# Optimization experiments

Measured on AMD Instinct MI355X. Metric: run time of the kernel, lower is better.

## Reference

```python
import jax, jax.numpy as jnp
import numpy as np

N = 50000        # nodes
E = 1600000      # edges
NFEAT = 128      # node feature dim
NEDGE = 16       # raw edge feature dim
NHID = 128
NLAYER = 4
NGRAPH = 512
NOUT = 128
BN_EPS = 1e-5


def _bn(h, g, b):
    # eval-mode BatchNorm1d with running_mean=0, running_var=1
    return h * (g / jnp.sqrt(1.0 + BN_EPS)) + b


def setup_inputs() -> dict:
    key = jax.random.key(0)
    ks = jax.random.split(key, 24)
    s = 0.05
    inp = {
        "x": jax.random.normal(ks[0], (N, NFEAT), jnp.float32),
        "edge_index": jax.random.randint(ks[1], (2, E), 0, N, jnp.int64),
        "edge_attr": jax.random.normal(ks[2], (E, NEDGE), jnp.float32),
        "batch": jnp.sort(jax.random.randint(ks[3], (N,), 0, NGRAPH, jnp.int64)),
        # input encoder MLP (Linear + BN + ReLU)
        "in_W": jax.random.normal(ks[4], (NFEAT, NHID), jnp.float32) * s,
        "in_b": jnp.zeros((NHID,), jnp.float32),
        "in_g": jnp.ones((NHID,), jnp.float32),
        "in_beta": jnp.zeros((NHID,), jnp.float32),
        # per-layer edge encoder MLPs
        "edge_W": jax.random.normal(ks[5], (NLAYER, NEDGE, NHID), jnp.float32) * s,
        "edge_b": jnp.zeros((NLAYER, NHID), jnp.float32),
        "edge_g": jnp.ones((NLAYER, NHID), jnp.float32),
        "edge_beta": jnp.zeros((NLAYER, NHID), jnp.float32),
        # per-layer GINEConv linear (bias=False since bn=True) and eps
        "conv_W": jax.random.normal(ks[6], (NLAYER, NHID, NHID), jnp.float32) * s,
        "eps": jnp.zeros((NLAYER,), jnp.float32),
        # per-layer BatchNorm after conv
        "bn_g": jnp.ones((NLAYER, NHID), jnp.float32),
        "bn_b": jnp.zeros((NLAYER, NHID), jnp.float32),
        # output encoder: 2-layer MLP, norm after layer 1, no final activation
        "out_W1": jax.random.normal(ks[7], (NHID, NHID), jnp.float32) * s,
        "out_b1": jnp.zeros((NHID,), jnp.float32),
        "out_g1": jnp.ones((NHID,), jnp.float32),
        "out_beta1": jnp.zeros((NHID,), jnp.float32),
        "out_W2": jax.random.normal(ks[8], (NHID, NOUT), jnp.float32) * s,
        "out_b2": jnp.zeros((NOUT,), jnp.float32),
    }
    return inp


def reference(x, edge_index, edge_attr, batch,
              in_W, in_b, in_g, in_beta,
              edge_W, edge_b, edge_g, edge_beta,
              conv_W, eps, bn_g, bn_b,
              out_W1, out_b1, out_g1, out_beta1,
              out_W2, out_b2):
    # input encoder (MLP, 1 layer: Linear + BN + ReLU)
    h = jax.nn.relu(_bn(x @ in_W + in_b, in_g, in_beta))
    prev = h
    src, dst = edge_index[0], edge_index[1]
    for l in range(NLAYER):
        # edge encoder
        ea = jax.nn.relu(_bn(edge_attr @ edge_W[l] + edge_b[l], edge_g[l], edge_beta[l]))
        # GINEConv: messages relu(x_src + e), sum-aggregate to dst
        m = jax.nn.relu(h[src] + ea)                         # [E, NHID]
        agg = jax.ops.segment_sum(m, dst, num_segments=N)    # [N, NHID]
        h = ((1.0 + eps[l]) * h + agg) @ conv_W[l]
        h = jax.nn.relu(_bn(h, bn_g[l], bn_b[l]))            # dropout=0
        h = h + prev                                         # residual
        prev = h
    # add pooling over graphs
    pooled = jax.ops.segment_sum(h, batch, num_segments=NGRAPH)  # [NGRAPH, NHID]
    # output encoder: Linear+BN+ReLU, then Linear
    o = jax.nn.relu(_bn(pooled @ out_W1 + out_b1, out_g1, out_beta1))
    return o @ out_W2 + out_b2
```

## Files before the change

kernel.cpp:

```cpp
#include <hip/hip_runtime.h>
#include <stdint.h>

typedef uint32_t u32;
typedef _Float16 h2v __attribute__((ext_vector_type(2)));
typedef __attribute__((ext_vector_type(8))) short bf16x8;
typedef __attribute__((ext_vector_type(8))) _Float16 f16x8_t;
typedef __attribute__((ext_vector_type(4))) float f32x4;

#define NGRAPH 512

__device__ __forceinline__ float uif(u32 u) { return __builtin_bit_cast(float, u); }
__device__ __forceinline__ u32 fiu(float f) { return __builtin_bit_cast(u32, f); }
__device__ __forceinline__ unsigned short bf16r(float f) {
    return (unsigned short)((fiu(f) + 0x8000u) >> 16);
}
__device__ __forceinline__ u32 pack_bf16(float lo, float hi) {
    return ((fiu(lo) + 0x8000u) >> 16) | ((fiu(hi) + 0x8000u) & 0xFFFF0000u);
}
__device__ __forceinline__ u32 pkh(float a, float b) {
    unsigned short la = __builtin_bit_cast(unsigned short, (_Float16)a);
    unsigned short hb = __builtin_bit_cast(unsigned short, (_Float16)b);
    return (u32)la | ((u32)hb << 16);
}

__global__ __launch_bounds__(256) void prep_kernel(
    const float* __restrict__ in_b, const float* __restrict__ in_g, const float* __restrict__ in_beta,
    const float* __restrict__ edge_b, const float* __restrict__ edge_g, const float* __restrict__ edge_beta,
    const float* __restrict__ bn_g, const float* __restrict__ bn_b,
    const float* __restrict__ out_b1, const float* __restrict__ out_g1, const float* __restrict__ out_beta1,
    float* __restrict__ consts)
{
    int c = threadIdx.x;
    if (c >= 128) return;
    const float rs = rsqrtf(1.0f + 1e-5f);
    float es = in_g[c] * rs;
    consts[c]       = es;
    consts[128 + c] = in_b[c] * es + in_beta[c];
    for (int l = 0; l < 4; ++l) {
        float s = edge_g[l*128 + c] * rs;
        consts[256  + l*128 + c] = s;
        consts[768  + l*128 + c] = edge_b[l*128 + c] * s + edge_beta[l*128 + c];
        float bs = bn_g[l*128 + c] * rs;
        consts[1280 + l*128 + c] = bs;
        consts[1792 + l*128 + c] = bn_b[l*128 + c];
    }
    float s1 = out_g1[c] * rs;
    consts[2304 + c] = s1;
    consts[2432 + c] = out_b1[c] * s1 + out_beta1[c];
}

__global__ __launch_bounds__(256) void wfrag_kernel(
    const float* __restrict__ edge_W, _Float16* __restrict__ wfrag)
{
    int idx = blockIdx.x*blockDim.x + threadIdx.x;
    if (idx >= 4*8*64*8) return;
    int j = idx & 7, lane = (idx >> 3) & 63, t = (idx >> 9) & 7, l = idx >> 12;
    int k = (lane >> 4)*8 + j;
    int n = t*16 + (lane & 15);
    wfrag[idx] = (k < 16) ? (_Float16)edge_W[(l*16 + k)*128 + n] : (_Float16)0.f;
}

__global__ __launch_bounds__(256) void prepw_kernel(
    const float* __restrict__ in_W, const float* __restrict__ conv_W,
    unsigned short* __restrict__ WtAll)
{
    for (int idx = blockIdx.x*blockDim.x + threadIdx.x; idx < 5*128*128;
         idx += gridDim.x*blockDim.x) {
        int w = idx >> 14, rem = idx & 16383;
        int nn = rem >> 7, kk = rem & 127;
        const float* S = (w == 0) ? in_W : conv_W + (size_t)(w-1)*16384;
        WtAll[idx] = bf16r(S[kk*128 + nn]);
    }
}

__global__ __launch_bounds__(256) void xconv_kernel(
    const float* __restrict__ x, u32* __restrict__ x16, int n4)
{
    for (int i = blockIdx.x*blockDim.x + threadIdx.x; i < n4;
         i += gridDim.x*blockDim.x) {
        float4 v = *(const float4*)(x + (size_t)i*4);
        uint2 o; o.x = pack_bf16(v.x, v.y); o.y = pack_bf16(v.z, v.w);
        *(uint2*)(x16 + (size_t)i*2) = o;
    }
}

__global__ __launch_bounds__(256) void count_kernel(
    const int* __restrict__ dst, int E, int* __restrict__ cnt)
{
    for (int e = blockIdx.x*blockDim.x + threadIdx.x; e < E; e += gridDim.x*blockDim.x)
        atomicAdd(&cnt[dst[e]], 1);
}

__global__ __launch_bounds__(1024) void scan_kernel(
    const int* __restrict__ cnt, int n, int E,
    int* __restrict__ offs, int* __restrict__ cursor)
{
    __shared__ int sh[1024];
    const int t = threadIdx.x;
    const int chunk = (n + 1023) >> 10;
    const int lo = t * chunk;
    const int hi = min(n, lo + chunk);
    int s = 0;
    for (int i = lo; i < hi; ++i) s += cnt[i];
    sh[t] = s;
    __syncthreads();
    for (int d = 1; d < 1024; d <<= 1) {
        int v = (t >= d) ? sh[t - d] : 0;
        __syncthreads();
        sh[t] += v;
        __syncthreads();
    }
    int base = sh[t] - s;
    for (int i = lo; i < hi; ++i) { int c = cnt[i]; offs[i] = base; cursor[i] = base; base += c; }
    if (t == 1023) offs[n] = E;
}

__global__ __launch_bounds__(256) void scatter_kernel(
    const int* __restrict__ src, const int* __restrict__ dst,
    const float* __restrict__ attr, int E,
    int* __restrict__ cursor, int* __restrict__ srcoff, uint4* __restrict__ attrp)
{
    const int T = gridDim.x * blockDim.x;
    const int tid = blockIdx.x*blockDim.x + threadIdx.x;
    int e[4]; int p[4];
    #pragma unroll
    for (int k = 0; k < 4; ++k) e[k] = tid + k*T;
    #pragma unroll
    for (int k = 0; k < 4; ++k)
        if (e[k] < E) p[k] = atomicAdd(&cursor[dst[e[k]]], 1);
    #pragma unroll
    for (int k = 0; k < 4; ++k) {
        if (e[k] >= E) continue;
        const int ee = e[k], pp = p[k];
        srcoff[pp] = src[ee] * 256;
        const float4* ar = (const float4*)(attr + (size_t)ee*16);
        float4 v0 = ar[0], v1 = ar[1], v2 = ar[2], v3 = ar[3];
        uint4 o0, o1;
        o0.x = pkh(v0.x, v0.y); o0.y = pkh(v0.z, v0.w);
        o0.z = pkh(v1.x, v1.y); o0.w = pkh(v1.z, v1.w);
        o1.x = pkh(v2.x, v2.y); o1.y = pkh(v2.z, v2.w);
        o1.z = pkh(v3.x, v3.y); o1.w = pkh(v3.z, v3.w);
        attrp[2*(size_t)pp] = o0; attrp[2*(size_t)pp + 1] = o1;
    }
}

__global__ __launch_bounds__(256) void goff_kernel(
    const int* __restrict__ batch, int n, int* __restrict__ goff)
{
    int g = blockIdx.x*blockDim.x + threadIdx.x;
    if (g > NGRAPH) return;
    if (g == NGRAPH) { goff[NGRAPH] = n; return; }
    int lo = 0, hi = n;
    while (lo < hi) { int m = (lo + hi) >> 1; if (batch[m] < g) lo = m + 1; else hi = m; }
    goff[g] = lo;
}

__global__ __launch_bounds__(256) void agg_kernel(
    const char* __restrict__ hb,
    const uint4* __restrict__ attrp,
    const int* __restrict__ srcoff,
    const int* __restrict__ offs,
    const _Float16* __restrict__ wfrag,
    const float* __restrict__ escale, const float* __restrict__ eoff,
    const float* __restrict__ epsp, int layer,
    u32* __restrict__ C16, int n)
{
    __shared__ float eabuf[4][128];
    const int wave = threadIdx.x >> 6, lane = threadIdx.x & 63;
    const int lane4 = lane * 4;
    const int c0 = lane * 2;
    const int l15 = lane & 15, l4 = lane >> 4;

    f16x8_t bw[8];
    #pragma unroll
    for (int t = 0; t < 8; ++t)
        bw[t] = *(const f16x8_t*)(wfrag + ((size_t)(layer*8 + t)*64 + lane)*8);
    float sc[8], of[8];
    #pragma unroll
    for (int t = 0; t < 8; ++t) {
        sc[t] = escale[l15 + 16*t];
        of[t] = eoff[l15 + 16*t];
    }
    const float epsv = 1.0f + epsp[layer];
    const f16x8_t az = (f16x8_t)(_Float16)0.f;

    for (int node = blockIdx.x*4 + wave; node < n; node += gridDim.x*4) {
        const int beg = offs[node], end = offs[node+1];

        float easum[8];
        #pragma unroll
        for (int t = 0; t < 8; ++t) easum[t] = 0.f;
        for (int g = beg; g < end; g += 16) {
            const int rem = end - g;
            f16x8_t a = az;
            if (l4 < 2) {
                int e = g + l15; if (e > end - 1) e = end - 1;
                a = *(const f16x8_t*)((const char*)attrp + (size_t)e*32 + l4*16);
            }
            if (rem >= 16) {
                #pragma unroll
                for (int t = 0; t < 8; ++t) {
                    f32x4 d = __builtin_amdgcn_mfma_f32_16x16x32_f16(
                        a, bw[t], f32x4{0.f,0.f,0.f,0.f}, 0, 0, 0);
                    #pragma unroll
                    for (int r = 0; r < 4; ++r)
                        easum[t] += fmaxf(fmaf(d[r], sc[t], of[t]), 0.f);
                }
            } else {
                #pragma unroll
                for (int t = 0; t < 8; ++t) {
                    f32x4 d = __builtin_amdgcn_mfma_f32_16x16x32_f16(
                        a, bw[t], f32x4{0.f,0.f,0.f,0.f}, 0, 0, 0);
                    #pragma unroll
                    for (int r = 0; r < 4; ++r) {
                        float y = fmaxf(fmaf(d[r], sc[t], of[t]), 0.f);
                        easum[t] += ((l4*4 + r) < rem) ? y : 0.f;
                    }
                }
            }
        }
        #pragma unroll
        for (int t = 0; t < 8; ++t) {
            float v = easum[t];
            v += __shfl_xor(v, 16);
            v += __shfl_xor(v, 32);
            easum[t] = v;
        }
        if (l4 == 0) {
            #pragma unroll
            for (int t = 0; t < 8; ++t)
                eabuf[wave][t*16 + l15] = easum[t];
        }
        float2 ea2 = *(float2*)&eabuf[wave][c0];

        float acc0 = ea2.x, acc1 = ea2.y;
        auto hedge = [&](int idx) {
            const int iu = __builtin_amdgcn_readfirstlane(idx);
            const u32 hv = *(const u32*)(hb + srcoff[iu] + lane4);
            acc0 += uif(hv << 16);
            acc1 += uif(hv & 0xFFFF0000u);
        };
        int i = beg;
        for (; i + 1 < end; i += 2) { hedge(i); hedge(i + 1); }
        if (i < end) hedge(i);

        const u32 hn = *(const u32*)(hb + (size_t)node*256 + lane4);
        float t0 = fmaf(epsv, uif(hn << 16), acc0);
        float t1 = fmaf(epsv, uif(hn & 0xFFFF0000u), acc1);
        C16[(size_t)node*64 + lane] = pack_bf16(t0, t1);
    }
}

__global__ __launch_bounds__(256) void conv_mfma_kernel(
    const unsigned short* X16, int M,
    const unsigned short* __restrict__ Wt,
    const float* __restrict__ scale, const float* __restrict__ off,
    const unsigned short* __restrict__ resid16,
    unsigned short* out16, int do_relu)
{
    __shared__ unsigned short Ws[128*128];
    for (int i = threadIdx.x*8; i < 128*128; i += 256*8) {
        int row = i >> 7;
        int bo = (i & 127) * 2;
        int4 v = *(const int4*)(Wt + i);
        *(int4*)((char*)Ws + row*256 + (bo ^ ((row & 7) << 4))) = v;
    }
    __syncthreads();
    const int wave = threadIdx.x >> 6, lane = threadIdx.x & 63;
    const int row0 = blockIdx.x*64 + wave*16;
    const int l15 = lane & 15, l4 = lane >> 4;
    int arow = row0 + l15; if (arow > M-1) arow = M-1;
    const unsigned short* ap = X16 + (size_t)arow*128 + l4*8;
    f32x4 acc[8];
    #pragma unroll
    for (int t = 0; t < 8; ++t) acc[t] = f32x4{0.f, 0.f, 0.f, 0.f};
    #pragma unroll
    for (int ks = 0; ks < 4; ++ks) {
        bf16x8 a = *(const bf16x8*)(ap + ks*32);
        #pragma unroll
        for (int t = 0; t < 8; ++t) {
            int brow = t*16 + l15;
            int bo = ks*64 + l4*16;
            bf16x8 b = *(const bf16x8*)((const char*)Ws + brow*256 + (bo ^ ((brow & 7) << 4)));
            acc[t] = __builtin_amdgcn_mfma_f32_16x16x32_bf16(a, b, acc[t], 0, 0, 0);
        }
    }
    #pragma unroll
    for (int t = 0; t < 8; ++t) {
        int col = t*16 + l15;
        float sc = scale[col], of = off[col];
        #pragma unroll
        for (int r = 0; r < 4; ++r) {
            int row = row0 + l4*4 + r;
            if (row < M) {
                float y = fmaf(acc[t][r], sc, of);
                if (do_relu) y = fmaxf(y, 0.f);
                if (resid16) y += uif((u32)resid16[(size_t)row*128 + col] << 16);
                out16[(size_t)row*128 + col] = bf16r(y);
            }
        }
    }
}

__global__ __launch_bounds__(256) void pool_kernel(
    const u32* __restrict__ h16, const int* __restrict__ goff,
    float* __restrict__ pooled)
{
    const int wave = threadIdx.x >> 6, lane = threadIdx.x & 63;
    const int g = blockIdx.x*4 + wave;
    if (g >= NGRAPH) return;
    float ax = 0.f, ay = 0.f;
    const int beg = goff[g], end = goff[g+1];
    for (int node = beg; node < end; ++node) {
        u32 v = h16[(size_t)node*64 + lane];
        ax += uif(v << 16); ay += uif(v & 0xFFFF0000u);
    }
    *(float2*)&pooled[g*128 + lane*2] = make_float2(ax, ay);
}

__global__ __launch_bounds__(256) void gemm128_kernel(
    const float* __restrict__ in, int rows,
    const float* __restrict__ W,
    const float* __restrict__ scale, const float* __restrict__ off,
    float* out, int do_relu)
{
    __shared__ float Wsh[128*128];
    for (int i = threadIdx.x*4; i < 128*128; i += 256*4)
        *(float4*)&Wsh[i] = *(const float4*)&W[i];
    __syncthreads();
    const int wave = threadIdx.x >> 6, lane = threadIdx.x & 63;
    const int c0 = lane * 2;
    const float sc0 = scale ? scale[c0]   : 1.0f;
    const float sc1 = scale ? scale[c0+1] : 1.0f;
    const float of0 = off ? off[c0]   : 0.0f;
    const float of1 = off ? off[c0+1] : 0.0f;
    for (int rp = blockIdx.x*4 + wave; rp*2 < rows; rp += gridDim.x*4) {
        const int row0 = __builtin_amdgcn_readfirstlane(rp * 2);
        const float* xr = in + (size_t)row0 * 128;
        float a00 = 0.f, a01 = 0.f, a10 = 0.f, a11 = 0.f;
        #pragma unroll 8
        for (int k = 0; k < 128; ++k) {
            float x0 = xr[k];
            float x1 = xr[128 + k];
            float2 w = *(const float2*)&Wsh[k*128 + c0];
            a00 = fmaf(x0, w.x, a00); a01 = fmaf(x0, w.y, a01);
            a10 = fmaf(x1, w.x, a10); a11 = fmaf(x1, w.y, a11);
        }
        float y00 = fmaf(a00, sc0, of0), y01 = fmaf(a01, sc1, of1);
        float y10 = fmaf(a10, sc0, of0), y11 = fmaf(a11, sc1, of1);
        if (do_relu) {
            y00 = fmaxf(y00, 0.f); y01 = fmaxf(y01, 0.f);
            y10 = fmaxf(y10, 0.f); y11 = fmaxf(y11, 0.f);
        }
        *(float2*)&out[(size_t)row0*128 + c0]     = make_float2(y00, y01);
        *(float2*)&out[(size_t)(row0+1)*128 + c0] = make_float2(y10, y11);
    }
}

extern "C" void kernel_launch(void* const* d_in, const int* in_sizes, int n_in,
                              void* d_out, int out_size, void* d_ws, size_t ws_size,
                              hipStream_t stream)
{
    const float* x         = (const float*)d_in[0];
    const int*   eidx      = (const int*)d_in[1];
    const float* eattr     = (const float*)d_in[2];
    const int*   batch     = (const int*)d_in[3];
    const float* in_W      = (const float*)d_in[4];
    const float* in_b      = (const float*)d_in[5];
    const float* in_g      = (const float*)d_in[6];
    const float* in_beta   = (const float*)d_in[7];
    const float* edge_W    = (const float*)d_in[8];
    const float* edge_b    = (const float*)d_in[9];
    const float* edge_g    = (const float*)d_in[10];
    const float* edge_beta = (const float*)d_in[11];
    const float* conv_W    = (const float*)d_in[12];
    const float* epsp      = (const float*)d_in[13];
    const float* bn_g      = (const float*)d_in[14];
    const float* bn_b      = (const float*)d_in[15];
    const float* out_W1    = (const float*)d_in[16];
    const float* out_b1    = (const float*)d_in[17];
    const float* out_g1    = (const float*)d_in[18];
    const float* out_beta1 = (const float*)d_in[19];
    const float* out_W2    = (const float*)d_in[20];
    const float* out_b2    = (const float*)d_in[21];

    const int N = in_sizes[0] / 128;
    const int E = in_sizes[1] / 2;
    const int* src = eidx;
    const int* dst = eidx + E;

    char* ws = (char*)d_ws;
    size_t o = 0;
    auto alloc = [&](size_t bytes) { void* p = ws + o; o = (o + bytes + 255) & ~(size_t)255; return p; };
    unsigned short* P    = (unsigned short*)alloc((size_t)N * 128 * 2);
    unsigned short* Q    = (unsigned short*)alloc((size_t)N * 128 * 2);
    uint4* attrp         = (uint4*)alloc((size_t)E * 32);
    int*   srcoff        = (int*)alloc((size_t)E * 4);
    int*   offs          = (int*)alloc((size_t)(N + 1) * 4);
    int*   cursor        = (int*)alloc((size_t)N * 4);
    int*   cnt           = (int*)alloc((size_t)N * 4);
    int*   goff          = (int*)alloc((NGRAPH + 1) * 4);
    float* pooled        = (float*)alloc(NGRAPH * 128 * 4);
    float* o1            = (float*)alloc(NGRAPH * 128 * 4);
    float* consts        = (float*)alloc(2560 * 4);
    _Float16* wfrag      = (_Float16*)alloc(4 * 8 * 64 * 8 * 2);
    unsigned short* WtAll = (unsigned short*)alloc(5 * 128 * 128 * 2);

    prep_kernel<<<1, 256, 0, stream>>>(in_b, in_g, in_beta,
                                       edge_b, edge_g, edge_beta,
                                       bn_g, bn_b, out_b1, out_g1, out_beta1,
                                       consts);
    wfrag_kernel<<<64, 256, 0, stream>>>(edge_W, wfrag);
    prepw_kernel<<<80, 256, 0, stream>>>(in_W, conv_W, WtAll);
    xconv_kernel<<<2048, 256, 0, stream>>>(x, (u32*)Q, N * 32);

    (void)hipMemsetAsync(cnt, 0, (size_t)N * 4, stream);
    count_kernel<<<2048, 256, 0, stream>>>(dst, E, cnt);
    scan_kernel<<<1, 1024, 0, stream>>>(cnt, N, E, offs, cursor);
    scatter_kernel<<<2048, 256, 0, stream>>>(src, dst, eattr, E, cursor, srcoff, attrp);
    goff_kernel<<<3, 256, 0, stream>>>(batch, N, goff);

    const int gblocks = (N + 63) / 64;
    conv_mfma_kernel<<<gblocks, 256, 0, stream>>>(Q, N, WtAll,
                                                  consts, consts + 128,
                                                  nullptr, Q, 1);

    unsigned short* cur = Q;
    unsigned short* oth = P;
    for (int l = 0; l < 4; ++l) {
        agg_kernel<<<2048, 256, 0, stream>>>((const char*)cur, attrp, srcoff, offs,
                                             wfrag,
                                             consts + 256 + l*128,
                                             consts + 768 + l*128,
                                             epsp, l, (u32*)oth, N);
        conv_mfma_kernel<<<gblocks, 256, 0, stream>>>(oth, N,
                                                      WtAll + (size_t)(1 + l)*16384,
                                                      consts + 1280 + l*128,
                                                      consts + 1792 + l*128,
                                                      cur, oth, 1);
        unsigned short* t = cur; cur = oth; oth = t;
    }

    pool_kernel<<<128, 256, 0, stream>>>((const u32*)cur, goff, pooled);

    gemm128_kernel<<<64, 256, 0, stream>>>(pooled, NGRAPH, out_W1,
                                           consts + 2304, consts + 2432, o1, 1);
    gemm128_kernel<<<64, 256, 0, stream>>>(o1, NGRAPH, out_W2,
                                           nullptr, out_b2, (float*)d_out, 0);
}
```

Baseline: 970.7 us.

## Precompute all four layers' edge-encoder aggregates once, then gather-only per layer

```diff
diff --git a/kernel.cpp b/kernel.cpp
--- a/kernel.cpp
+++ b/kernel.cpp
@@ -50,14 +50,18 @@
 }
 
 __global__ __launch_bounds__(256) void wfrag_kernel(
-    const float* __restrict__ edge_W, _Float16* __restrict__ wfrag)
+    const float* __restrict__ edge_W, const float* __restrict__ edge_g,
+    _Float16* __restrict__ wfrag)
 {
     int idx = blockIdx.x*blockDim.x + threadIdx.x;
     if (idx >= 4*8*64*8) return;
     int j = idx & 7, lane = (idx >> 3) & 63, t = (idx >> 9) & 7, l = idx >> 12;
     int k = (lane >> 4)*8 + j;
     int n = t*16 + (lane & 15);
-    wfrag[idx] = (k < 16) ? (_Float16)edge_W[(l*16 + k)*128 + n] : (_Float16)0.f;
+    const float rs = rsqrtf(1.0f + 1e-5f);
+    wfrag[idx] = (k < 16)
+        ? (_Float16)(edge_W[(l*16 + k)*128 + n] * (edge_g[l*128 + n] * rs))
+        : (_Float16)0.f;
 }
 
 __global__ __launch_bounds__(256) void prepw_kernel(
@@ -155,41 +159,34 @@
     goff[g] = lo;
 }
 
-__global__ __launch_bounds__(256) void agg_kernel(
-    const char* __restrict__ hb,
-    const uint4* __restrict__ attrp,
-    const int* __restrict__ srcoff,
-    const int* __restrict__ offs,
-    const _Float16* __restrict__ wfrag,
-    const float* __restrict__ escale, const float* __restrict__ eoff,
-    const float* __restrict__ epsp, int layer,
-    u32* __restrict__ C16, int n)
+__global__ __launch_bounds__(256) void eagg4_kernel(
+    const uint4* __restrict__ attrp, const int* __restrict__ offs,
+    const _Float16* __restrict__ wfrag, const float* __restrict__ consts,
+    u32* __restrict__ eagg, int n)
 {
     __shared__ float eabuf[4][128];
     const int wave = threadIdx.x >> 6, lane = threadIdx.x & 63;
-    const int lane4 = lane * 4;
     const int c0 = lane * 2;
     const int l15 = lane & 15, l4 = lane >> 4;
 
-    f16x8_t bw[8];
-    #pragma unroll
-    for (int t = 0; t < 8; ++t)
-        bw[t] = *(const f16x8_t*)(wfrag + ((size_t)(layer*8 + t)*64 + lane)*8);
-    float sc[8], of[8];
-    #pragma unroll
-    for (int t = 0; t < 8; ++t) {
-        sc[t] = escale[l15 + 16*t];
-        of[t] = eoff[l15 + 16*t];
-    }
-    const float epsv = 1.0f + epsp[layer];
+    f16x8_t bw[32];
+    #pragma unroll
+    for (int lt = 0; lt < 32; ++lt)
+        bw[lt] = *(const f16x8_t*)(wfrag + ((size_t)lt*64 + lane)*8);
+    float of[32];
+    #pragma unroll
+    for (int l = 0; l < 4; ++l)
+        #pragma unroll
+        for (int t = 0; t < 8; ++t)
+            of[l*8 + t] = consts[768 + l*128 + t*16 + l15];
     const f16x8_t az = (f16x8_t)(_Float16)0.f;
 
     for (int node = blockIdx.x*4 + wave; node < n; node += gridDim.x*4) {
         const int beg = offs[node], end = offs[node+1];
-
-        float easum[8];
+        float easum[32];
         #pragma unroll
-        for (int t = 0; t < 8; ++t) easum[t] = 0.f;
+        for (int lt = 0; lt < 32; ++lt) easum[lt] = 0.f;
+
         for (int g = beg; g < end; g += 16) {
             const int rem = end - g;
             f16x8_t a = az;
@@ -199,54 +196,96 @@
             }
             if (rem >= 16) {
                 #pragma unroll
-                for (int t = 0; t < 8; ++t) {
+                for (int lt = 0; lt < 32; ++lt) {
                     f32x4 d = __builtin_amdgcn_mfma_f32_16x16x32_f16(
-                        a, bw[t], f32x4{0.f,0.f,0.f,0.f}, 0, 0, 0);
+                        a, bw[lt], f32x4{0.f,0.f,0.f,0.f}, 0, 0, 0);
                     #pragma unroll
                     for (int r = 0; r < 4; ++r)
-                        easum[t] += fmaxf(fmaf(d[r], sc[t], of[t]), 0.f);
+                        easum[lt] += fmaxf(d[r] + of[lt], 0.f);
                 }
             } else {
                 #pragma unroll
-                for (int t = 0; t < 8; ++t) {
+                for (int lt = 0; lt < 32; ++lt) {
                     f32x4 d = __builtin_amdgcn_mfma_f32_16x16x32_f16(
-                        a, bw[t], f32x4{0.f,0.f,0.f,0.f}, 0, 0, 0);
+                        a, bw[lt], f32x4{0.f,0.f,0.f,0.f}, 0, 0, 0);
                     #pragma unroll
                     for (int r = 0; r < 4; ++r) {
-                        float y = fmaxf(fmaf(d[r], sc[t], of[t]), 0.f);
-                        easum[t] += ((l4*4 + r) < rem) ? y : 0.f;
+                        float y = fmaxf(d[r] + of[lt], 0.f);
+                        easum[lt] += ((l4*4 + r) < rem) ? y : 0.f;
                     }
                 }
             }
         }
         #pragma unroll
-        for (int t = 0; t < 8; ++t) {
-            float v = easum[t];
-            v += __shfl_xor(v, 16);
-            v += __shfl_xor(v, 32);
-            easum[t] = v;
-        }
-        if (l4 == 0) {
+        for (int l = 0; l < 4; ++l) {
             #pragma unroll
-            for (int t = 0; t < 8; ++t)
-                eabuf[wave][t*16 + l15] = easum[t];
-        }
-        float2 ea2 = *(float2*)&eabuf[wave][c0];
-
-        float acc0 = ea2.x, acc1 = ea2.y;
-        auto hedge = [&](int idx) {
-            const int iu = __builtin_amdgcn_readfirstlane(idx);
-            const u32 hv = *(const u32*)(hb + srcoff[iu] + lane4);
-            acc0 += uif(hv << 16);
-            acc1 += uif(hv & 0xFFFF0000u);
-        };
+            for (int t = 0; t < 8; ++t) {
+                float v = easum[l*8 + t];
+                v += __shfl_xor(v, 16);
+                v += __shfl_xor(v, 32);
+                if (l4 == 0) eabuf[wave][t*16 + l15] = v;
+            }
+            float2 ea2 = *(float2*)&eabuf[wave][c0];
+            eagg[(size_t)l*n*64 + (size_t)node*64 + lane] = pack_bf16(ea2.x, ea2.y);
+        }
+    }
+}
+
+__global__ __launch_bounds__(256) void hagg_kernel(
+    const char* __restrict__ hb, const int* __restrict__ srcoff,
+    const int* __restrict__ offs, const u32* __restrict__ eagg_l,
+    const float* __restrict__ epsp, int layer,
+    u32* __restrict__ C16, int n)
+{
+    const int wave = threadIdx.x >> 6, lane = threadIdx.x & 63;
+    const int lane4 = lane * 4;
+    const float epsv = 1.0f + epsp[layer];
+    for (int node = blockIdx.x*4 + wave; node < n; node += gridDim.x*4) {
+        const int beg = offs[node], end = offs[node+1];
+        float acc0 = 0.f, acc1 = 0.f;
         int i = beg;
-        for (; i + 1 < end; i += 2) { hedge(i); hedge(i + 1); }
-        if (i < end) hedge(i);
-
+        for (; i + 7 < end; i += 8) {
+            const int iu = __builtin_amdgcn_readfirstlane(i);
+            const int4 sa = *(const int4*)(srcoff + iu);
+            const int4 sb = *(const int4*)(srcoff + iu + 4);
+            const u32 h0 = *(const u32*)(hb + sa.x + lane4);
+            const u32 h1 = *(const u32*)(hb + sa.y + lane4);
+            const u32 h2 = *(const u32*)(hb + sa.z + lane4);
+            const u32 h3 = *(const u32*)(hb + sa.w + lane4);
+            const u32 h4 = *(const u32*)(hb + sb.x + lane4);
+            const u32 h5 = *(const u32*)(hb + sb.y + lane4);
+            const u32 h6 = *(const u32*)(hb + sb.z + lane4);
+            const u32 h7 = *(const u32*)(hb + sb.w + lane4);
+            acc0 += uif(h0 << 16); acc1 += uif(h0 & 0xFFFF0000u);
+            acc0 += uif(h1 << 16); acc1 += uif(h1 & 0xFFFF0000u);
+            acc0 += uif(h2 << 16); acc1 += uif(h2 & 0xFFFF0000u);
+            acc0 += uif(h3 << 16); acc1 += uif(h3 & 0xFFFF0000u);
+            acc0 += uif(h4 << 16); acc1 += uif(h4 & 0xFFFF0000u);
+            acc0 += uif(h5 << 16); acc1 += uif(h5 & 0xFFFF0000u);
+            acc0 += uif(h6 << 16); acc1 += uif(h6 & 0xFFFF0000u);
+            acc0 += uif(h7 << 16); acc1 += uif(h7 & 0xFFFF0000u);
+        }
+        for (; i + 3 < end; i += 4) {
+            const int iu = __builtin_amdgcn_readfirstlane(i);
+            const int4 sa = *(const int4*)(srcoff + iu);
+            const u32 h0 = *(const u32*)(hb + sa.x + lane4);
+            const u32 h1 = *(const u32*)(hb + sa.y + lane4);
+            const u32 h2 = *(const u32*)(hb + sa.z + lane4);
+            const u32 h3 = *(const u32*)(hb + sa.w + lane4);
+            acc0 += uif(h0 << 16); acc1 += uif(h0 & 0xFFFF0000u);
+            acc0 += uif(h1 << 16); acc1 += uif(h1 & 0xFFFF0000u);
+            acc0 += uif(h2 << 16); acc1 += uif(h2 & 0xFFFF0000u);
+            acc0 += uif(h3 << 16); acc1 += uif(h3 & 0xFFFF0000u);
+        }
+        for (; i < end; ++i) {
+            const int iu = __builtin_amdgcn_readfirstlane(i);
+            const u32 h0 = *(const u32*)(hb + srcoff[iu] + lane4);
+            acc0 += uif(h0 << 16); acc1 += uif(h0 & 0xFFFF0000u);
+        }
+        const u32 eg = eagg_l[(size_t)node*64 + lane];
         const u32 hn = *(const u32*)(hb + (size_t)node*256 + lane4);
-        float t0 = fmaf(epsv, uif(hn << 16), acc0);
-        float t1 = fmaf(epsv, uif(hn & 0xFFFF0000u), acc1);
+        float t0 = fmaf(epsv, uif(hn << 16),          acc0 + uif(eg << 16));
+        float t1 = fmaf(epsv, uif(hn & 0xFFFF0000u),  acc1 + uif(eg & 0xFFFF0000u));
         C16[(size_t)node*64 + lane] = pack_bf16(t0, t1);
     }
 }
@@ -396,6 +435,7 @@
     unsigned short* Q    = (unsigned short*)alloc((size_t)N * 128 * 2);
     uint4* attrp         = (uint4*)alloc((size_t)E * 32);
     int*   srcoff        = (int*)alloc((size_t)E * 4);
+    u32*   eagg          = (u32*)alloc((size_t)N * 64 * 4 * 4);
     int*   offs          = (int*)alloc((size_t)(N + 1) * 4);
     int*   cursor        = (int*)alloc((size_t)N * 4);
     int*   cnt           = (int*)alloc((size_t)N * 4);
@@ -410,7 +450,7 @@
                                        edge_b, edge_g, edge_beta,
                                        bn_g, bn_b, out_b1, out_g1, out_beta1,
                                        consts);
-    wfrag_kernel<<<64, 256, 0, stream>>>(edge_W, wfrag);
+    wfrag_kernel<<<64, 256, 0, stream>>>(edge_W, edge_g, wfrag);
     prepw_kernel<<<80, 256, 0, stream>>>(in_W, conv_W, WtAll);
     xconv_kernel<<<2048, 256, 0, stream>>>(x, (u32*)Q, N * 32);
 
@@ -424,15 +464,14 @@
     conv_mfma_kernel<<<gblocks, 256, 0, stream>>>(Q, N, WtAll,
                                                   consts, consts + 128,
                                                   nullptr, Q, 1);
+    eagg4_kernel<<<2048, 256, 0, stream>>>(attrp, offs, wfrag, consts, eagg, N);
 
     unsigned short* cur = Q;
     unsigned short* oth = P;
     for (int l = 0; l < 4; ++l) {
-        agg_kernel<<<2048, 256, 0, stream>>>((const char*)cur, attrp, srcoff, offs,
-                                             wfrag,
-                                             consts + 256 + l*128,
-                                             consts + 768 + l*128,
-                                             epsp, l, (u32*)oth, N);
+        hagg_kernel<<<2048, 256, 0, stream>>>((const char*)cur, srcoff, offs,
+                                              eagg + (size_t)l * N * 64,
+                                              epsp, l, (u32*)oth, N);
         conv_mfma_kernel<<<gblocks, 256, 0, stream>>>(oth, N,
                                                       WtAll + (size_t)(1 + l)*16384,
                                                       consts + 1280 + l*128,
```

New measurement: 1.031 ms. 1.06x slower.
